# Optimization experiments

Measured on AMD Instinct MI355X. Metric: run time of the kernel, lower is better.

The kernel has to match this reference:

```python
import jax, jax.numpy as jnp
import numpy as np

# MANO prior contact vertex indices (f1+f2+f3+f4+f5+f0 from CMap_loss3)
_F1 = [697,698,699,700,712,713,714,715,737,738,739,740,741,743,744,745,746,748,749,750,753,754,755,756,757,758,759,760,761,762,763,764,765,766,767,768]
_F2 = [46,47,48,49,164,165,166,167,194,195,223,237,238,280,281,298,301,317,320,323,324,325,326,327,328,329,330,331,332,333,340,341,342,343,344,345,346,347,348,349,350,351,352,353,354,355]
_F3 = [356,357,358,359,375,376,386,387,396,397,402,403,413,429,433,434,435,436,437,438,439,440,441,442,443,444,452,453,454,455,456,459,460,461,462,463,464,465,466,467]
_F4 = [468,469,470,471,484,485,486,496,497,506,507,513,514,524,545,546,547,548,549,550,551,552,553,555,563,564,565,566,567,570,572,573,574,575,576,577,578]
_F5 = [580,581,582,583,600,601,602,614,615,624,625,630,631,641,663,664,665,666,667,668,670,672,680,681,682,683,684,686,687,688,689,690,691,692,693,694,695]
_F0 = [73,96,98,99,772,774,775,777]
PRIOR_IDX = np.array(_F1 + _F2 + _F3 + _F4 + _F5 + _F0, dtype=np.int32)


def _sqdist(a, b):
    # a: [B,N,3], b: [B,M,3] -> squared distances [B,N,M] via ||a||^2+||b||^2-2ab
    a2 = jnp.sum(a * a, -1)          # [B,N]
    b2 = jnp.sum(b * b, -1)          # [B,M]
    ab = jnp.einsum('bnd,bmd->bnm', a, b)
    return jnp.maximum(a2[:, :, None] + b2[:, None, :] - 2.0 * ab, 0.0)


def _knn1(src, trg):
    # nearest neighbor (K=1): squared dists + indices, like pytorch3d knn_points
    d2 = _sqdist(src, trg)           # [B,N,M]
    return jnp.min(d2, -1), jnp.argmin(d2, -1)


def _verts_normals(verts, faces):
    # area-weighted vertex normals (pytorch3d verts_normals_packed)
    v0 = verts[:, faces[:, 0]]       # [B,F,3]
    v1 = verts[:, faces[:, 1]]
    v2 = verts[:, faces[:, 2]]
    fn = jnp.cross(v1 - v0, v2 - v0)
    vn = jnp.zeros_like(verts)
    vn = vn.at[:, faces[:, 0]].add(fn).at[:, faces[:, 1]].add(fn).at[:, faces[:, 2]].add(fn)
    return vn / (jnp.linalg.norm(vn, axis=-1, keepdims=True) + 1e-12)


def setup_inputs() -> dict:
    key = jax.random.key(0)
    ks = jax.random.split(key, 8)
    B, N1, V, F, Z, P = 64, 8192, 778, 1538, 64, 61
    scale = 0.1  # keep points in a 0.1 box so contact thresholds (0.005/0.01) fire
    return {
        'obj_xyz': jax.random.uniform(ks[0], (B, N1, 3), jnp.float32) * scale,
        'recon_xyz': jax.random.uniform(ks[1], (B, V, 3), jnp.float32) * scale,
        'gt_xyz': jax.random.uniform(ks[2], (B, V, 3), jnp.float32) * scale,
        'mean': jax.random.normal(ks[3], (B, Z), jnp.float32),
        'log_var': jax.random.normal(ks[4], (B, Z), jnp.float32),
        'recon_param': jax.random.normal(ks[5], (B, P), jnp.float32),
        'x_param': jax.random.normal(ks[6], (B, P), jnp.float32),
        'faces': jax.random.randint(ks[7], (F, 3), 0, V, jnp.int32),
    }


def reference(obj_xyz, recon_xyz, gt_xyz, mean, log_var, recon_param, x_param, faces):
    B = obj_xyz.shape[0]
    fB = jnp.float32(B)

    # KNN from object points to gt / reconstructed hand (squared dists)
    d_gt, _ = _knn1(obj_xyz, gt_xyz)            # [B,N1]
    d_rec, idx_rec = _knn1(obj_xyz, recon_xyz)  # [B,N1], [B,N1]

    # param loss: MSE sum / B
    param_loss = jnp.sum((recon_param - x_param) ** 2) / fB

    # CVAE loss: chamfer (point_reduction='sum', batch_reduction='mean') + KLD
    d2 = _sqdist(recon_xyz, gt_xyz)             # [B,778,778]
    recon_loss = jnp.mean(jnp.sum(jnp.min(d2, -1), -1)) + jnp.mean(jnp.sum(jnp.min(d2, -2), -1))
    KLD = -0.5 * jnp.sum(1.0 + log_var - mean ** 2 - jnp.exp(log_var)) / fB * 10.0
    cvae_loss = recon_loss + KLD

    # CMap_loss3: obj NN distance to prior hand contact verts, masked by cmap
    cmap = d_rec < 0.01 ** 2                    # [B,N1] bool
    prior = recon_xyz[:, PRIOR_IDX, :]          # [B,222,3]
    obj_CD, _ = _knn1(obj_xyz, prior)           # [B,N1]
    n_points = jnp.sum(cmap).astype(jnp.float32)
    cmap_loss = 3000.0 * jnp.sum(jnp.where(cmap, obj_CD, 0.0)) / (fB * n_points)

    # CMap consistency: contact-map overlap ratio
    recon_cmap = jnp.sqrt(d_rec) < 0.005
    gt_cmap = jnp.sqrt(d_gt) < 0.005
    gt_cnum = jnp.sum(gt_cmap).astype(jnp.float32) + 0.0001
    consistency_loss = -5.0 * jnp.sum(recon_cmap & gt_cmap).astype(jnp.float32) / gt_cnum

    # inter-penetration: gather NN hand verts/normals, sign of dot, masked dist sum
    vn = _verts_normals(recon_xyz, faces)                               # [B,778,3]
    nn_v = jnp.take_along_axis(recon_xyz, idx_rec[..., None], axis=1)   # [B,N1,3]
    nn_n = jnp.take_along_axis(vn, idx_rec[..., None], axis=1)          # [B,N1,3]
    interior = jnp.sum((nn_v - obj_xyz) * nn_n, -1) > 0                 # [B,N1]
    penetr_loss = 100.0 * jnp.sum(jnp.where(interior, d_rec, 0.0)) / fB

    a, b, c, d, e = 1.0, 0.1, 1000.0, 10.0, 10.0
    loss = a * cvae_loss + b * param_loss + c * cmap_loss + d * consistency_loss + e * penetr_loss
    return loss
```

## Files before the change

kernel.cpp:

```cpp
#include <hip/hip_runtime.h>
#include <math.h>

#define NB     64
#define N1V    8192
#define NPTS   (NB * N1V)
#define NV     778
#define NVP    780
#define NQ     195
#define SEG1Q  51
#define NFACE  1538
#define NZ     64
#define NPAR   61
#define NPRIOR 204
#define PPT    8
#define BIAS   0.0625f

#define GT_BLOCKS  256
#define REC_BLOCKS 256
#define CH_BLOCKS  128
#define NROLE_BLOCKS (GT_BLOCKS + REC_BLOCKS + CH_BLOCKS)

#define PREP_BLOCKS 193

#define BATCH_F4 2352
#define ACC_OFF   (NB * BATCH_F4 * 4)
#define FLAGS_OFF (ACC_OFF + 16)
#define GC_OFF    (FLAGS_OFF + 256)

static constexpr int PRIOR_LIST[NPRIOR] = {
  697,698,699,700,712,713,714,715,737,738,739,740,741,743,744,745,746,748,749,750,
  753,754,755,756,757,758,759,760,761,762,763,764,765,766,767,768,
  46,47,48,49,164,165,166,167,194,195,223,237,238,280,281,298,301,317,320,323,
  324,325,326,327,328,329,330,331,332,333,340,341,342,343,344,345,346,347,348,349,
  350,351,352,353,354,355,
  356,357,358,359,375,376,386,387,396,397,402,403,413,429,433,434,435,436,437,438,
  439,440,441,442,443,444,452,453,454,455,456,459,460,461,462,463,464,465,466,467,
  468,469,470,471,484,485,486,496,497,506,507,513,514,524,545,546,547,548,549,550,
  551,552,553,555,563,564,565,566,567,570,572,573,574,575,576,577,578,
  580,581,582,583,600,601,602,614,615,624,625,630,631,641,663,664,665,666,667,668,
  670,672,680,681,682,683,684,686,687,688,689,690,691,692,693,694,695,
  73,96,98,99,772,774,775,777
};

struct PermT { unsigned short v[NV]; };
static constexpr PermT make_perm() {
    PermT t{};
    bool mem[NV] = {};
    for (int i = 0; i < NPRIOR; ++i) mem[PRIOR_LIST[i]] = true;
    int a = 0, b = NPRIOR;
    for (int j = 0; j < NV; ++j) {
        if (mem[j]) t.v[a++] = (unsigned short)j;
        else        t.v[b++] = (unsigned short)j;
    }
    return t;
}
__device__ __constant__ PermT c_perm = make_perm();

__global__ __launch_bounds__(256) void k_prep(const float* __restrict__ recon,
                                              const float* __restrict__ gt,
                                              const int* __restrict__ faces,
                                              const float* __restrict__ mean,
                                              const float* __restrict__ log_var,
                                              const float* __restrict__ rp,
                                              const float* __restrict__ xp,
                                              float4* __restrict__ ws4,
                                              float* __restrict__ acc,
                                              unsigned int* __restrict__ flags) {
    int blk = blockIdx.x, tid = threadIdx.x;

    if (blk == 192) {
        flags[tid] = 0u;
        __shared__ float sp[2];
        if (tid < 2) sp[tid] = 0.0f;
        __syncthreads();
        float s_param = 0.0f, s_kld = 0.0f;
        for (int i = tid; i < NB * NPAR; i += 256) {
            float d = rp[i] - xp[i];
            s_param += d * d;
        }
        for (int i = tid; i < NB * NZ; i += 256) {
            float mv = mean[i], lv = log_var[i];
            s_kld += 1.0f + lv - mv * mv - expf(lv);
        }
        atomicAdd(&sp[0], s_param);
        atomicAdd(&sp[1], s_kld);
        __syncthreads();
        if (tid == 0) { acc[8] = sp[0]; acc[9] = sp[1]; }
        return;
    }

    int b = blk & 63, role = blk >> 6;
    float4* gt4   = ws4 + (size_t)b * BATCH_F4;
    float4* rec4p = gt4 + NVP;
    float4* nrm4p = rec4p + NVP;

    if (role == 0) {
        if (b == 0 && tid < 8) acc[tid] = 0.0f;
        if (b == 0 && tid == 15) acc[15] = 0.0f;
        const float* gb = gt + (size_t)b * NV * 3;
        for (int j = tid; j < NV; j += 256) {
            float x = gb[3*j], y = gb[3*j+1], z = gb[3*j+2];
            gt4[j] = make_float4(x, y, z, x*x + y*y + z*z);
        }
        if (tid < 2) gt4[NV + tid] = make_float4(0.f, 0.f, 0.f, 1e30f);
        return;
    }

    if (role == 1) {
        const float* rb = recon + (size_t)b * NV * 3;
        for (int j = tid; j < NVP; j += 256) {
            if (j < NV) {
                int src = c_perm.v[j];
                float x = rb[3*src], y = rb[3*src+1], z = rb[3*src+2];
                rec4p[j] = make_float4(x, y, z, x*x + y*y + z*z + BIAS);
            } else {
                rec4p[j] = make_float4(0.f, 0.f, 0.f, 1e30f);
            }
        }
        return;
    }

    {
        __shared__ float s_x[NV], s_y[NV], s_z[NV];
        __shared__ float s_vnx[NV], s_vny[NV], s_vnz[NV];
        const float* rb = recon + (size_t)b * NV * 3;
        for (int j = tid; j < NV; j += 256) {
            s_x[j] = rb[3*j]; s_y[j] = rb[3*j+1]; s_z[j] = rb[3*j+2];
            s_vnx[j] = 0.0f; s_vny[j] = 0.0f; s_vnz[j] = 0.0f;
        }
        __syncthreads();
        for (int f = tid; f < NFACE; f += 256) {
            int i0 = faces[3*f], i1 = faces[3*f+1], i2 = faces[3*f+2];
            float p0x = s_x[i0], p0y = s_y[i0], p0z = s_z[i0];
            float e1x = s_x[i1] - p0x, e1y = s_y[i1] - p0y, e1z = s_z[i1] - p0z;
            float e2x = s_x[i2] - p0x, e2y = s_y[i2] - p0y, e2z = s_z[i2] - p0z;
            float fx = e1y * e2z - e1z * e2y;
            float fy = e1z * e2x - e1x * e2z;
            float fz = e1x * e2y - e1y * e2x;
            atomicAdd(&s_vnx[i0], fx); atomicAdd(&s_vny[i0], fy); atomicAdd(&s_vnz[i0], fz);
            atomicAdd(&s_vnx[i1], fx); atomicAdd(&s_vny[i1], fy); atomicAdd(&s_vnz[i1], fz);
            atomicAdd(&s_vnx[i2], fx); atomicAdd(&s_vny[i2], fy); atomicAdd(&s_vnz[i2], fz);
        }
        __syncthreads();
        for (int j = tid; j < NVP; j += 256) {
            if (j < NV) {
                int src = c_perm.v[j];
                nrm4p[j] = make_float4(s_vnx[src], s_vny[src], s_vnz[src], 0.0f);
            } else {
                nrm4p[j] = make_float4(0.f, 0.f, 1.f, 0.0f);
            }
        }
    }
}

#define LOAD_PTS(ob)                                                          \
    const float4* ob4 = (const float4*)((ob) + (size_t)tid * 24);             \
    float4 q0 = ob4[0], q1 = ob4[1], q2 = ob4[2],                             \
           q3 = ob4[3], q4 = ob4[4], q5 = ob4[5];                             \
    float px[PPT], py[PPT], pz[PPT];                                          \
    px[0]=q0.x; py[0]=q0.y; pz[0]=q0.z;  px[1]=q0.w; py[1]=q1.x; pz[1]=q1.y;  \
    px[2]=q1.z; py[2]=q1.w; pz[2]=q2.x;  px[3]=q2.y; py[3]=q2.z; pz[3]=q2.w;  \
    px[4]=q3.x; py[4]=q3.y; pz[4]=q3.z;  px[5]=q3.w; py[5]=q4.x; pz[5]=q4.y;  \
    px[6]=q4.z; py[6]=q4.w; pz[6]=q5.x;  px[7]=q5.y; py[7]=q5.z; pz[7]=q5.w;

__device__ __forceinline__ void spin_wait(unsigned int* f, int tid) {
    if (tid == 0) {
        while (__hip_atomic_load(f, __ATOMIC_ACQUIRE, __HIP_MEMORY_SCOPE_AGENT) == 0u)
            __builtin_amdgcn_s_sleep(2);
    }
    __syncthreads();
}

__global__ __launch_bounds__(256) void k_fused(const float* __restrict__ obj,
                                               const float4* __restrict__ ws4,
                                               float* __restrict__ acc,
                                               unsigned int* __restrict__ flags,
                                               unsigned char* __restrict__ gcA,
                                               float* __restrict__ out) {
    __shared__ float4 s_t[NVP];
    __shared__ float s_red[4];
    __shared__ unsigned int s_tk;
    int tid = threadIdx.x;
    int blk = blockIdx.x;

    if (blk < GT_BLOCKS) {
        int r = blk;
        int b = r >> 2, chunk = r & 3;
        const float4* gt4v = ws4 + (size_t)b * BATCH_F4;
        for (int j = tid; j < NVP; j += 256) s_t[j] = gt4v[j];
        if (tid == 0) s_red[0] = 0.0f;
        __syncthreads();

        const float* ob = obj + ((size_t)b * N1V + (size_t)chunk * 2048) * 3;
        LOAD_PTS(ob)
        float nax[PPT], nay[PPT], naz[PPT], mgt[PPT];
#pragma unroll
        for (int i = 0; i < PPT; ++i) {
            nax[i] = -2.0f * px[i]; nay[i] = -2.0f * py[i]; naz[i] = -2.0f * pz[i];
            mgt[i] = 3.4e38f;
        }
#pragma unroll 1
        for (int jq = 0; jq < NQ; ++jq) {
            int j = 4 * jq;
            float4 t0 = s_t[j], t1 = s_t[j+1], t2 = s_t[j+2], t3 = s_t[j+3];
#pragma unroll
            for (int i = 0; i < PPT; ++i) {
                float d0 = fmaf(nax[i], t0.x, fmaf(nay[i], t0.y, fmaf(naz[i], t0.z, t0.w)));
                float d1 = fmaf(nax[i], t1.x, fmaf(nay[i], t1.y, fmaf(naz[i], t1.z, t1.w)));
                float d2 = fmaf(nax[i], t2.x, fmaf(nay[i], t2.y, fmaf(naz[i], t2.z, t2.w)));
                float d3 = fmaf(nax[i], t3.x, fmaf(nay[i], t3.y, fmaf(naz[i], t3.z, t3.w)));
                mgt[i] = fminf(fminf(mgt[i], fminf(d0, d1)), fminf(d2, d3));
            }
        }
        float lN_gt = 0.0f;
        unsigned int gcbits = 0;
#pragma unroll
        for (int i = 0; i < PPT; ++i) {
            float a2 = px[i]*px[i] + py[i]*py[i] + pz[i]*pz[i];
            float dgt = fmaxf(a2 + mgt[i], 0.0f);
            if (sqrtf(dgt) < 0.005f) { lN_gt += 1.0f; gcbits |= (1u << i); }
        }
        gcA[(size_t)r * 256 + tid] = (unsigned char)gcbits;
        atomicAdd(&s_red[0], lN_gt);
        __syncthreads();
        if (tid == 0) {
            __threadfence();
            __hip_atomic_store(&flags[r], 1u, __ATOMIC_RELEASE, __HIP_MEMORY_SCOPE_AGENT);
            atomicAdd(&acc[5], s_red[0]);
        }
    } else if (blk < GT_BLOCKS + REC_BLOCKS) {
        int r = blk - GT_BLOCKS;
        int b = r >> 2, chunk = r & 3;
        const float4* base = ws4 + (size_t)b * BATCH_F4;
        const float4* rec4p = base + NVP;
        const float4* nrm4p = base + 2 * NVP;
        for (int j = tid; j < NVP; j += 256) s_t[j] = rec4p[j];
        if (tid < 4) s_red[tid] = 0.0f;
        __syncthreads();

        const float* ob = obj + ((size_t)b * N1V + (size_t)chunk * 2048) * 3;
        LOAD_PTS(ob)
        float nax[PPT], nay[PPT], naz[PPT], m[PPT];
        int q[PPT];
#pragma unroll
        for (int i = 0; i < PPT; ++i) {
            nax[i] = -2.0f * px[i]; nay[i] = -2.0f * py[i]; naz[i] = -2.0f * pz[i];
            m[i] = 3.4e38f; q[i] = 0;
        }
        float mp[PPT];
#pragma unroll 1
        for (int jq = 0; jq < SEG1Q; ++jq) {
            int j = 4 * jq;
            float4 t0 = s_t[j], t1 = s_t[j+1], t2 = s_t[j+2], t3 = s_t[j+3];
#pragma unroll
            for (int i = 0; i < PPT; ++i) {
                float d0 = fmaf(nax[i], t0.x, fmaf(nay[i], t0.y, fmaf(naz[i], t0.z, t0.w)));
                float d1 = fmaf(nax[i], t1.x, fmaf(nay[i], t1.y, fmaf(naz[i], t1.z, t1.w)));
                float d2 = fmaf(nax[i], t2.x, fmaf(nay[i], t2.y, fmaf(naz[i], t2.z, t2.w)));
                float d3 = fmaf(nax[i], t3.x, fmaf(nay[i], t3.y, fmaf(naz[i], t3.z, t3.w)));
                float mn = fminf(fminf(fminf(d0, d1), fminf(d2, d3)), m[i]);
                q[i] = (mn < m[i]) ? jq : q[i];
                m[i] = mn;
            }
        }
#pragma unroll
        for (int i = 0; i < PPT; ++i) mp[i] = m[i];
#pragma unroll 1
        for (int jq = SEG1Q; jq < NQ; ++jq) {
            int j = 4 * jq;
            float4 t0 = s_t[j], t1 = s_t[j+1], t2 = s_t[j+2], t3 = s_t[j+3];
#pragma unroll
            for (int i = 0; i < PPT; ++i) {
                float d0 = fmaf(nax[i], t0.x, fmaf(nay[i], t0.y, fmaf(naz[i], t0.z, t0.w)));
                float d1 = fmaf(nax[i], t1.x, fmaf(nay[i], t1.y, fmaf(naz[i], t1.z, t1.w)));
                float d2 = fmaf(nax[i], t2.x, fmaf(nay[i], t2.y, fmaf(naz[i], t2.z, t2.w)));
                float d3 = fmaf(nax[i], t3.x, fmaf(nay[i], t3.y, fmaf(naz[i], t3.z, t3.w)));
                float mn = fminf(fminf(fminf(d0, d1), fminf(d2, d3)), m[i]);
                q[i] = (mn < m[i]) ? jq : q[i];
                m[i] = mn;
            }
        }
        float lS_cmap = 0.0f, lN_cmap = 0.0f, lS_pen = 0.0f;
        unsigned int rcbits = 0;
#pragma unroll
        for (int i = 0; i < PPT; ++i) {
            float a2 = px[i]*px[i] + py[i]*py[i] + pz[i]*pz[i];
            float drec = fmaxf(a2 + (m[i]  - BIAS), 0.0f);
            float dpri = fmaxf(a2 + (mp[i] - BIAS), 0.0f);
            bool cm = drec < 1e-4f;
            bool rc = sqrtf(drec) < 0.005f;
            if (cm) { lS_cmap += dpri; lN_cmap += 1.0f; }
            if (rc) rcbits |= (1u << i);
            int jr = 4 * q[i];
            float4 t0 = s_t[jr], t1 = s_t[jr+1], t2 = s_t[jr+2], t3 = s_t[jr+3];
            float d0 = fmaf(nax[i], t0.x, fmaf(nay[i], t0.y, fmaf(naz[i], t0.z, t0.w)));
            float d1 = fmaf(nax[i], t1.x, fmaf(nay[i], t1.y, fmaf(naz[i], t1.z, t1.w)));
            float d2 = fmaf(nax[i], t2.x, fmaf(nay[i], t2.y, fmaf(naz[i], t2.z, t2.w)));
            float d3 = fmaf(nax[i], t3.x, fmaf(nay[i], t3.y, fmaf(naz[i], t3.z, t3.w)));
            float mmin = fminf(fminf(d0, d1), fminf(d2, d3));
            int off = (d0 == mmin) ? 0 : ((d1 == mmin) ? 1 : ((d2 == mmin) ? 2 : 3));
            int jstar = jr + off;
            float4 tS = s_t[jstar];
            float4 nr = nrm4p[jstar];
            float ddot = (tS.x - px[i]) * nr.x + (tS.y - py[i]) * nr.y
                       + (tS.z - pz[i]) * nr.z;
            if (ddot > 0.0f) lS_pen += drec;
        }
        atomicAdd(&s_red[0], lS_cmap);
        atomicAdd(&s_red[1], lN_cmap);
        atomicAdd(&s_red[2], lS_pen);
        spin_wait(&flags[r], tid);
        unsigned int gcb = gcA[(size_t)r * 256 + tid];
        float lcons = (float)__popc(rcbits & gcb);
        atomicAdd(&s_red[3], lcons);
        __syncthreads();
        if (tid == 0) atomicAdd(&acc[3], s_red[0]);
        if (tid == 1) atomicAdd(&acc[4], s_red[1]);
        if (tid == 2) atomicAdd(&acc[7], s_red[2]);
        if (tid == 3) atomicAdd(&acc[6], s_red[3]);
    } else {
        int c   = blk - (GT_BLOCKS + REC_BLOCKS);
        int b   = c >> 1;
        int dir = c & 1;
        const float4* base = ws4 + (size_t)b * BATCH_F4;
        const float4* srcv = dir ? base : (base + NVP);
        const float4* tgtv = dir ? (base + NVP) : base;
        for (int j = tid; j < NVP; j += 256) s_t[j] = tgtv[j];
        if (tid == 0) s_red[0] = 0.0f;
        __syncthreads();

        const int CPT = 4;
        float nax[CPT], nay[CPT], naz[CPT], a2[CPT], m[CPT];
        bool valid[CPT];
#pragma unroll
        for (int k = 0; k < CPT; ++k) {
            int p = tid + 256 * k;
            valid[k] = (p < NV);
            float4 s = srcv[valid[k] ? p : 0];
            nax[k] = -2.0f * s.x; nay[k] = -2.0f * s.y; naz[k] = -2.0f * s.z;
            a2[k] = s.w;
            m[k] = 3.4e38f;
        }
#pragma unroll 1
        for (int j = 0; j < NVP; j += 4) {
            float4 t0 = s_t[j], t1 = s_t[j+1], t2 = s_t[j+2], t3 = s_t[j+3];
#pragma unroll
            for (int k = 0; k < CPT; ++k) {
                float d0 = fmaf(nax[k], t0.x, fmaf(nay[k], t0.y, fmaf(naz[k], t0.z, t0.w)));
                float d1 = fmaf(nax[k], t1.x, fmaf(nay[k], t1.y, fmaf(naz[k], t1.z, t1.w)));
                float d2 = fmaf(nax[k], t2.x, fmaf(nay[k], t2.y, fmaf(naz[k], t2.z, t2.w)));
                float d3 = fmaf(nax[k], t3.x, fmaf(nay[k], t3.y, fmaf(naz[k], t3.z, t3.w)));
                m[k] = fminf(fminf(m[k], fminf(d0, d1)), fminf(d2, d3));
            }
        }
        float local = 0.0f;
#pragma unroll
        for (int k = 0; k < CPT; ++k)
            if (valid[k]) local += fmaxf(a2[k] + m[k] - BIAS, 0.0f);
        atomicAdd(&s_red[0], local);
        __syncthreads();
        if (tid == 0) atomicAdd(&acc[2], s_red[0]);
    }

    __syncthreads();
    if (tid == 0) {
        __threadfence();
        s_tk = atomicAdd((unsigned int*)&acc[15], 1u);
    }
    __syncthreads();
    if (s_tk == NROLE_BLOCKS - 1 && tid == 0) {
        __threadfence();
        const float fB = 64.0f;
        float a2v = __hip_atomic_load(&acc[2], __ATOMIC_RELAXED, __HIP_MEMORY_SCOPE_AGENT);
        float a3  = __hip_atomic_load(&acc[3], __ATOMIC_RELAXED, __HIP_MEMORY_SCOPE_AGENT);
        float a4  = __hip_atomic_load(&acc[4], __ATOMIC_RELAXED, __HIP_MEMORY_SCOPE_AGENT);
        float a5  = __hip_atomic_load(&acc[5], __ATOMIC_RELAXED, __HIP_MEMORY_SCOPE_AGENT);
        float a6  = __hip_atomic_load(&acc[6], __ATOMIC_RELAXED, __HIP_MEMORY_SCOPE_AGENT);
        float a7  = __hip_atomic_load(&acc[7], __ATOMIC_RELAXED, __HIP_MEMORY_SCOPE_AGENT);
        float a8  = __hip_atomic_load(&acc[8], __ATOMIC_RELAXED, __HIP_MEMORY_SCOPE_AGENT);
        float a9  = __hip_atomic_load(&acc[9], __ATOMIC_RELAXED, __HIP_MEMORY_SCOPE_AGENT);
        float param_loss  = a8 / fB;
        float KLD         = -0.5f * a9 / fB * 10.0f;
        float recon_loss  = a2v / fB;
        float cmap_loss   = 3000.0f * a3 / (fB * a4);
        float consistency = -5.0f * a6 / (a5 + 0.0001f);
        float penetr      = 100.0f * a7 / fB;
        out[0] = (recon_loss + KLD) + 0.1f * param_loss + 1000.0f * cmap_loss
               + 10.0f * consistency + 10.0f * penetr;
    }
}

extern "C" void kernel_launch(void* const* d_in, const int* in_sizes, int n_in,
                              void* d_out, int out_size, void* d_ws, size_t ws_size,
                              hipStream_t stream) {
    (void)in_sizes; (void)n_in; (void)out_size; (void)ws_size;
    const float* obj     = (const float*)d_in[0];
    const float* recon   = (const float*)d_in[1];
    const float* gt      = (const float*)d_in[2];
    const float* mean    = (const float*)d_in[3];
    const float* log_var = (const float*)d_in[4];
    const float* rp      = (const float*)d_in[5];
    const float* xp      = (const float*)d_in[6];
    const int*   faces   = (const int*)d_in[7];
    float* wsf = (float*)d_ws;
    float4* ws4 = (float4*)d_ws;
    float* acc = wsf + ACC_OFF;
    unsigned int* flags = (unsigned int*)(wsf + FLAGS_OFF);
    unsigned char* gcA  = (unsigned char*)(wsf + GC_OFF);
    float* out = (float*)d_out;

    k_prep <<<PREP_BLOCKS,  256, 0, stream>>>(recon, gt, faces, mean, log_var,
                                              rp, xp, ws4, acc, flags);
    k_fused<<<NROLE_BLOCKS, 256, 0, stream>>>(obj, ws4, acc, flags, gcA, out);
}
```

Measured before the change: 189.7 us.

## Fuse prep kernel into main kernel with per-batch normal flags

Removes the separate prep kernel. Each scan block now builds its own float4 target table in shared memory straight from the raw inputs. Vertex normals are computed by 64 extra blocks in the same launch and published through per-batch release flags, which the recon blocks spin-wait on before the penetration pass. This removes one kernel launch and the workspace round trip, at the cost of redundant table construction per block and a memset launch to zero the counters and flags. The spin-waits could deadlock if the normal blocks are not scheduled, though they sit at high block indices.

```diff
diff --git a/kernel.cpp b/kernel.cpp
--- a/kernel.cpp
+++ b/kernel.cpp
@@ -18,14 +18,16 @@
 #define GT_BLOCKS  256
 #define REC_BLOCKS 256
 #define CH_BLOCKS  128
-#define NROLE_BLOCKS (GT_BLOCKS + REC_BLOCKS + CH_BLOCKS)
-
-#define PREP_BLOCKS 193
-
-#define BATCH_F4 2352
-#define ACC_OFF   (NB * BATCH_F4 * 4)
+#define NRM_BLOCKS 64
+#define REC_BASE GT_BLOCKS
+#define CH_BASE  (REC_BASE + REC_BLOCKS)
+#define NRM_BASE (CH_BASE + CH_BLOCKS)
+#define NBLOCKS  (NRM_BASE + NRM_BLOCKS)
+
+#define ACC_OFF   (NB * NVP * 4)
 #define FLAGS_OFF (ACC_OFF + 16)
-#define GC_OFF    (FLAGS_OFF + 256)
+#define NFLAGS    320
+#define GC_OFF    (FLAGS_OFF + NFLAGS)
 
 static constexpr int PRIOR_LIST[NPRIOR] = {
   697,698,699,700,712,713,714,715,737,738,739,740,741,743,744,745,746,748,749,750,
@@ -56,102 +58,9 @@
 }
 __device__ __constant__ PermT c_perm = make_perm();
 
-__global__ __launch_bounds__(256) void k_prep(const float* __restrict__ recon,
-                                              const float* __restrict__ gt,
-                                              const int* __restrict__ faces,
-                                              const float* __restrict__ mean,
-                                              const float* __restrict__ log_var,
-                                              const float* __restrict__ rp,
-                                              const float* __restrict__ xp,
-                                              float4* __restrict__ ws4,
-                                              float* __restrict__ acc,
-                                              unsigned int* __restrict__ flags) {
-    int blk = blockIdx.x, tid = threadIdx.x;
-
-    if (blk == 192) {
-        flags[tid] = 0u;
-        __shared__ float sp[2];
-        if (tid < 2) sp[tid] = 0.0f;
-        __syncthreads();
-        float s_param = 0.0f, s_kld = 0.0f;
-        for (int i = tid; i < NB * NPAR; i += 256) {
-            float d = rp[i] - xp[i];
-            s_param += d * d;
-        }
-        for (int i = tid; i < NB * NZ; i += 256) {
-            float mv = mean[i], lv = log_var[i];
-            s_kld += 1.0f + lv - mv * mv - expf(lv);
-        }
-        atomicAdd(&sp[0], s_param);
-        atomicAdd(&sp[1], s_kld);
-        __syncthreads();
-        if (tid == 0) { acc[8] = sp[0]; acc[9] = sp[1]; }
-        return;
-    }
-
-    int b = blk & 63, role = blk >> 6;
-    float4* gt4   = ws4 + (size_t)b * BATCH_F4;
-    float4* rec4p = gt4 + NVP;
-    float4* nrm4p = rec4p + NVP;
-
-    if (role == 0) {
-        if (b == 0 && tid < 8) acc[tid] = 0.0f;
-        if (b == 0 && tid == 15) acc[15] = 0.0f;
-        const float* gb = gt + (size_t)b * NV * 3;
-        for (int j = tid; j < NV; j += 256) {
-            float x = gb[3*j], y = gb[3*j+1], z = gb[3*j+2];
-            gt4[j] = make_float4(x, y, z, x*x + y*y + z*z);
-        }
-        if (tid < 2) gt4[NV + tid] = make_float4(0.f, 0.f, 0.f, 1e30f);
-        return;
-    }
-
-    if (role == 1) {
-        const float* rb = recon + (size_t)b * NV * 3;
-        for (int j = tid; j < NVP; j += 256) {
-            if (j < NV) {
-                int src = c_perm.v[j];
-                float x = rb[3*src], y = rb[3*src+1], z = rb[3*src+2];
-                rec4p[j] = make_float4(x, y, z, x*x + y*y + z*z + BIAS);
-            } else {
-                rec4p[j] = make_float4(0.f, 0.f, 0.f, 1e30f);
-            }
-        }
-        return;
-    }
-
-    {
-        __shared__ float s_x[NV], s_y[NV], s_z[NV];
-        __shared__ float s_vnx[NV], s_vny[NV], s_vnz[NV];
-        const float* rb = recon + (size_t)b * NV * 3;
-        for (int j = tid; j < NV; j += 256) {
-            s_x[j] = rb[3*j]; s_y[j] = rb[3*j+1]; s_z[j] = rb[3*j+2];
-            s_vnx[j] = 0.0f; s_vny[j] = 0.0f; s_vnz[j] = 0.0f;
-        }
-        __syncthreads();
-        for (int f = tid; f < NFACE; f += 256) {
-            int i0 = faces[3*f], i1 = faces[3*f+1], i2 = faces[3*f+2];
-            float p0x = s_x[i0], p0y = s_y[i0], p0z = s_z[i0];
-            float e1x = s_x[i1] - p0x, e1y = s_y[i1] - p0y, e1z = s_z[i1] - p0z;
-            float e2x = s_x[i2] - p0x, e2y = s_y[i2] - p0y, e2z = s_z[i2] - p0z;
-            float fx = e1y * e2z - e1z * e2y;
-            float fy = e1z * e2x - e1x * e2z;
-            float fz = e1x * e2y - e1y * e2x;
-            atomicAdd(&s_vnx[i0], fx); atomicAdd(&s_vny[i0], fy); atomicAdd(&s_vnz[i0], fz);
-            atomicAdd(&s_vnx[i1], fx); atomicAdd(&s_vny[i1], fy); atomicAdd(&s_vnz[i1], fz);
-            atomicAdd(&s_vnx[i2], fx); atomicAdd(&s_vny[i2], fy); atomicAdd(&s_vnz[i2], fz);
-        }
-        __syncthreads();
-        for (int j = tid; j < NVP; j += 256) {
-            if (j < NV) {
-                int src = c_perm.v[j];
-                nrm4p[j] = make_float4(s_vnx[src], s_vny[src], s_vnz[src], 0.0f);
-            } else {
-                nrm4p[j] = make_float4(0.f, 0.f, 1.f, 0.0f);
-            }
-        }
-    }
-}
+struct ScanSh { float4 t[NVP]; float red[4]; };
+struct NrmSh  { float x[NV], y[NV], z[NV], vnx[NV], vny[NV], vnz[NV]; };
+union ShU { ScanSh scan; NrmSh nrm; };
 
 #define LOAD_PTS(ob)                                                          \
     const float4* ob4 = (const float4*)((ob) + (size_t)tid * 24);             \
@@ -171,24 +80,31 @@
     __syncthreads();
 }
 
-__global__ __launch_bounds__(256) void k_fused(const float* __restrict__ obj,
-                                               const float4* __restrict__ ws4,
-                                               float* __restrict__ acc,
-                                               unsigned int* __restrict__ flags,
-                                               unsigned char* __restrict__ gcA,
-                                               float* __restrict__ out) {
-    __shared__ float4 s_t[NVP];
-    __shared__ float s_red[4];
+__global__ __launch_bounds__(256) void k_all(
+        const float* __restrict__ obj,   const float* __restrict__ recon,
+        const float* __restrict__ gt,    const int*   __restrict__ faces,
+        const float* __restrict__ mean,  const float* __restrict__ log_var,
+        const float* __restrict__ rp,    const float* __restrict__ xp,
+        float4* __restrict__ ws4,        float* __restrict__ acc,
+        unsigned int* __restrict__ flags, unsigned char* __restrict__ gcA,
+        float* __restrict__ out) {
+    __shared__ ShU sh;
     __shared__ unsigned int s_tk;
+    __shared__ float s_pk[2];
     int tid = threadIdx.x;
     int blk = blockIdx.x;
 
     if (blk < GT_BLOCKS) {
-        int r = blk;
-        int b = r >> 2, chunk = r & 3;
-        const float4* gt4v = ws4 + (size_t)b * BATCH_F4;
-        for (int j = tid; j < NVP; j += 256) s_t[j] = gt4v[j];
-        if (tid == 0) s_red[0] = 0.0f;
+        int r = blk, b = r >> 2, chunk = r & 3;
+        const float* gb = gt + (size_t)b * NV * 3;
+        float4* s_t = sh.scan.t;
+        for (int j = tid; j < NVP; j += 256) {
+            if (j < NV) {
+                float x = gb[3*j], y = gb[3*j+1], z = gb[3*j+2];
+                s_t[j] = make_float4(x, y, z, x*x + y*y + z*z);
+            } else s_t[j] = make_float4(0.f, 0.f, 0.f, 1e30f);
+        }
+        if (tid == 0) sh.scan.red[0] = 0.0f;
         __syncthreads();
 
         const float* ob = obj + ((size_t)b * N1V + (size_t)chunk * 2048) * 3;
@@ -221,21 +137,25 @@
             if (sqrtf(dgt) < 0.005f) { lN_gt += 1.0f; gcbits |= (1u << i); }
         }
         gcA[(size_t)r * 256 + tid] = (unsigned char)gcbits;
-        atomicAdd(&s_red[0], lN_gt);
+        atomicAdd(&sh.scan.red[0], lN_gt);
         __syncthreads();
         if (tid == 0) {
             __threadfence();
             __hip_atomic_store(&flags[r], 1u, __ATOMIC_RELEASE, __HIP_MEMORY_SCOPE_AGENT);
-            atomicAdd(&acc[5], s_red[0]);
-        }
-    } else if (blk < GT_BLOCKS + REC_BLOCKS) {
-        int r = blk - GT_BLOCKS;
-        int b = r >> 2, chunk = r & 3;
-        const float4* base = ws4 + (size_t)b * BATCH_F4;
-        const float4* rec4p = base + NVP;
-        const float4* nrm4p = base + 2 * NVP;
-        for (int j = tid; j < NVP; j += 256) s_t[j] = rec4p[j];
-        if (tid < 4) s_red[tid] = 0.0f;
+            atomicAdd(&acc[5], sh.scan.red[0]);
+        }
+    } else if (blk < CH_BASE) {
+        int r = blk - REC_BASE, b = r >> 2, chunk = r & 3;
+        const float* rb = recon + (size_t)b * NV * 3;
+        float4* s_t = sh.scan.t;
+        for (int j = tid; j < NVP; j += 256) {
+            if (j < NV) {
+                int src = c_perm.v[j];
+                float x = rb[3*src], y = rb[3*src+1], z = rb[3*src+2];
+                s_t[j] = make_float4(x, y, z, x*x + y*y + z*z + BIAS);
+            } else s_t[j] = make_float4(0.f, 0.f, 0.f, 1e30f);
+        }
+        if (tid < 4) sh.scan.red[tid] = 0.0f;
         __syncthreads();
 
         const float* ob = obj + ((size_t)b * N1V + (size_t)chunk * 2048) * 3;
@@ -280,8 +200,9 @@
                 m[i] = mn;
             }
         }
-        float lS_cmap = 0.0f, lN_cmap = 0.0f, lS_pen = 0.0f;
+        float lS_cmap = 0.0f, lN_cmap = 0.0f;
         unsigned int rcbits = 0;
+        int js[PPT]; float drecs[PPT];
 #pragma unroll
         for (int i = 0; i < PPT; ++i) {
             float a2 = px[i]*px[i] + py[i]*py[i] + pz[i]*pz[i];
@@ -299,34 +220,50 @@
             float d3 = fmaf(nax[i], t3.x, fmaf(nay[i], t3.y, fmaf(naz[i], t3.z, t3.w)));
             float mmin = fminf(fminf(d0, d1), fminf(d2, d3));
             int off = (d0 == mmin) ? 0 : ((d1 == mmin) ? 1 : ((d2 == mmin) ? 2 : 3));
-            int jstar = jr + off;
-            float4 tS = s_t[jstar];
-            float4 nr = nrm4p[jstar];
+            js[i] = jr + off;
+            drecs[i] = drec;
+        }
+        atomicAdd(&sh.scan.red[0], lS_cmap);
+        atomicAdd(&sh.scan.red[1], lN_cmap);
+        spin_wait(&flags[256 + b], tid);
+        spin_wait(&flags[r], tid);
+        const float4* nrm4p = ws4 + (size_t)b * NVP;
+        float lS_pen = 0.0f;
+#pragma unroll
+        for (int i = 0; i < PPT; ++i) {
+            float4 tS = s_t[js[i]];
+            float4 nr = nrm4p[js[i]];
             float ddot = (tS.x - px[i]) * nr.x + (tS.y - py[i]) * nr.y
                        + (tS.z - pz[i]) * nr.z;
-            if (ddot > 0.0f) lS_pen += drec;
-        }
-        atomicAdd(&s_red[0], lS_cmap);
-        atomicAdd(&s_red[1], lN_cmap);
-        atomicAdd(&s_red[2], lS_pen);
-        spin_wait(&flags[r], tid);
+            if (ddot > 0.0f) lS_pen += drecs[i];
+        }
         unsigned int gcb = gcA[(size_t)r * 256 + tid];
         float lcons = (float)__popc(rcbits & gcb);
-        atomicAdd(&s_red[3], lcons);
-        __syncthreads();
-        if (tid == 0) atomicAdd(&acc[3], s_red[0]);
-        if (tid == 1) atomicAdd(&acc[4], s_red[1]);
-        if (tid == 2) atomicAdd(&acc[7], s_red[2]);
-        if (tid == 3) atomicAdd(&acc[6], s_red[3]);
-    } else {
-        int c   = blk - (GT_BLOCKS + REC_BLOCKS);
+        atomicAdd(&sh.scan.red[2], lS_pen);
+        atomicAdd(&sh.scan.red[3], lcons);
+        __syncthreads();
+        if (tid == 0) atomicAdd(&acc[3], sh.scan.red[0]);
+        if (tid == 1) atomicAdd(&acc[4], sh.scan.red[1]);
+        if (tid == 2) atomicAdd(&acc[7], sh.scan.red[2]);
+        if (tid == 3) atomicAdd(&acc[6], sh.scan.red[3]);
+    } else if (blk < NRM_BASE) {
+        int c   = blk - CH_BASE;
         int b   = c >> 1;
         int dir = c & 1;
-        const float4* base = ws4 + (size_t)b * BATCH_F4;
-        const float4* srcv = dir ? base : (base + NVP);
-        const float4* tgtv = dir ? (base + NVP) : base;
-        for (int j = tid; j < NVP; j += 256) s_t[j] = tgtv[j];
-        if (tid == 0) s_red[0] = 0.0f;
+        const float* rb = recon + (size_t)b * NV * 3;
+        const float* gb = gt    + (size_t)b * NV * 3;
+        const float* tb = dir ? rb : gb;
+        const float* sb = dir ? gb : rb;
+        float4* s_t = sh.scan.t;
+        for (int j = tid; j < NVP; j += 256) {
+            if (j < NV) {
+                float x = tb[3*j], y = tb[3*j+1], z = tb[3*j+2];
+                float w = x*x + y*y + z*z;
+                if (dir) w += BIAS;
+                s_t[j] = make_float4(x, y, z, w);
+            } else s_t[j] = make_float4(0.f, 0.f, 0.f, 1e30f);
+        }
+        if (tid == 0) sh.scan.red[0] = 0.0f;
         __syncthreads();
 
         const int CPT = 4;
@@ -336,9 +273,12 @@
         for (int k = 0; k < CPT; ++k) {
             int p = tid + 256 * k;
             valid[k] = (p < NV);
-            float4 s = srcv[valid[k] ? p : 0];
-            nax[k] = -2.0f * s.x; nay[k] = -2.0f * s.y; naz[k] = -2.0f * s.z;
-            a2[k] = s.w;
+            int pp = valid[k] ? p : 0;
+            float x = sb[3*pp], y = sb[3*pp+1], z = sb[3*pp+2];
+            float w = x*x + y*y + z*z;
+            if (!dir) w += BIAS;
+            nax[k] = -2.0f * x; nay[k] = -2.0f * y; naz[k] = -2.0f * z;
+            a2[k] = w;
             m[k] = 3.4e38f;
         }
 #pragma unroll 1
@@ -357,18 +297,68 @@
 #pragma unroll
         for (int k = 0; k < CPT; ++k)
             if (valid[k]) local += fmaxf(a2[k] + m[k] - BIAS, 0.0f);
-        atomicAdd(&s_red[0], local);
-        __syncthreads();
-        if (tid == 0) atomicAdd(&acc[2], s_red[0]);
+        atomicAdd(&sh.scan.red[0], local);
+        __syncthreads();
+        if (tid == 0) atomicAdd(&acc[2], sh.scan.red[0]);
+    } else {
+        int b = blk - NRM_BASE;
+        const float* rb = recon + (size_t)b * NV * 3;
+        for (int j = tid; j < NV; j += 256) {
+            sh.nrm.x[j] = rb[3*j]; sh.nrm.y[j] = rb[3*j+1]; sh.nrm.z[j] = rb[3*j+2];
+            sh.nrm.vnx[j] = 0.0f; sh.nrm.vny[j] = 0.0f; sh.nrm.vnz[j] = 0.0f;
+        }
+        __syncthreads();
+        for (int f = tid; f < NFACE; f += 256) {
+            int i0 = faces[3*f], i1 = faces[3*f+1], i2 = faces[3*f+2];
+            float p0x = sh.nrm.x[i0], p0y = sh.nrm.y[i0], p0z = sh.nrm.z[i0];
+            float e1x = sh.nrm.x[i1] - p0x, e1y = sh.nrm.y[i1] - p0y, e1z = sh.nrm.z[i1] - p0z;
+            float e2x = sh.nrm.x[i2] - p0x, e2y = sh.nrm.y[i2] - p0y, e2z = sh.nrm.z[i2] - p0z;
+            float fx = e1y * e2z - e1z * e2y;
+            float fy = e1z * e2x - e1x * e2z;
+            float fz = e1x * e2y - e1y * e2x;
+            atomicAdd(&sh.nrm.vnx[i0], fx); atomicAdd(&sh.nrm.vny[i0], fy); atomicAdd(&sh.nrm.vnz[i0], fz);
+            atomicAdd(&sh.nrm.vnx[i1], fx); atomicAdd(&sh.nrm.vny[i1], fy); atomicAdd(&sh.nrm.vnz[i1], fz);
+            atomicAdd(&sh.nrm.vnx[i2], fx); atomicAdd(&sh.nrm.vny[i2], fy); atomicAdd(&sh.nrm.vnz[i2], fz);
+        }
+        __syncthreads();
+        float4* nrm4p = ws4 + (size_t)b * NVP;
+        for (int j = tid; j < NVP; j += 256) {
+            if (j < NV) {
+                int src = c_perm.v[j];
+                nrm4p[j] = make_float4(sh.nrm.vnx[src], sh.nrm.vny[src], sh.nrm.vnz[src], 0.0f);
+            } else nrm4p[j] = make_float4(0.f, 0.f, 1.f, 0.0f);
+        }
+        __syncthreads();
+        if (tid == 0) {
+            __threadfence();
+            __hip_atomic_store(&flags[256 + b], 1u, __ATOMIC_RELEASE, __HIP_MEMORY_SCOPE_AGENT);
+        }
+        if (b == 0) {
+            if (tid < 2) s_pk[tid] = 0.0f;
+            __syncthreads();
+            float s_param = 0.0f, s_kld = 0.0f;
+            for (int i = tid; i < NB * NPAR; i += 256) {
+                float d = rp[i] - xp[i];
+                s_param += d * d;
+            }
+            for (int i = tid; i < NB * NZ; i += 256) {
+                float mv = mean[i], lv = log_var[i];
+                s_kld += 1.0f + lv - mv * mv - expf(lv);
+            }
+            atomicAdd(&s_pk[0], s_param);
+            atomicAdd(&s_pk[1], s_kld);
+            __syncthreads();
+            if (tid == 0) { atomicAdd(&acc[8], s_pk[0]); atomicAdd(&acc[9], s_pk[1]); }
+        }
     }
 
     __syncthreads();
     if (tid == 0) {
-        __threadfence();
+        asm volatile("s_waitcnt vmcnt(0)" ::: "memory");
         s_tk = atomicAdd((unsigned int*)&acc[15], 1u);
     }
     __syncthreads();
-    if (s_tk == NROLE_BLOCKS - 1 && tid == 0) {
+    if (s_tk == NBLOCKS - 1 && tid == 0) {
         __threadfence();
         const float fB = 64.0f;
         float a2v = __hip_atomic_load(&acc[2], __ATOMIC_RELAXED, __HIP_MEMORY_SCOPE_AGENT);
@@ -409,7 +399,7 @@
     unsigned char* gcA  = (unsigned char*)(wsf + GC_OFF);
     float* out = (float*)d_out;
 
-    k_prep <<<PREP_BLOCKS,  256, 0, stream>>>(recon, gt, faces, mean, log_var,
-                                              rp, xp, ws4, acc, flags);
-    k_fused<<<NROLE_BLOCKS, 256, 0, stream>>>(obj, ws4, acc, flags, gcA, out);
+    hipMemsetAsync(acc, 0, (16 + NFLAGS) * sizeof(float), stream);
+    k_all<<<NBLOCKS, 256, 0, stream>>>(obj, recon, gt, faces, mean, log_var,
+                                       rp, xp, ws4, acc, flags, gcA, out);
 }
```

Result: faster. 167.4 us (-11.7%).
